# Performance work log

Hardware: AMD Instinct MI355X
Metric: run time of the kernel (lower is better)

The kernel has to match this reference:

```python
import jax, jax.numpy as jnp
import numpy as np

B, T, D = 2, 2048, 2048
H, HKV, HD = 16, 4, 128
I = 5632
EPS = 1e-5


def setup_inputs() -> dict:
    ks = jax.random.split(jax.random.key(0), 12)
    s = 0.02
    return {
        "x": jax.random.normal(ks[0], (B, T, D), jnp.float32),
        "rope_cos": jax.random.uniform(ks[1], (T, HD // 2), jnp.float32),
        "rope_sin": jax.random.uniform(ks[2], (T, HD // 2), jnp.float32),
        "ln1_w": jnp.ones((D,), jnp.float32),
        "ln2_w": jnp.ones((D,), jnp.float32),
        "wq_w": jax.random.normal(ks[3], (D, H * HD), jnp.float32) * s,
        "wq_b": jnp.zeros((H * HD,), jnp.float32),
        "wk_w": jax.random.normal(ks[4], (D, HKV * HD), jnp.float32) * s,
        "wk_b": jnp.zeros((HKV * HD,), jnp.float32),
        "wv_w": jax.random.normal(ks[5], (D, HKV * HD), jnp.float32) * s,
        "wv_b": jnp.zeros((HKV * HD,), jnp.float32),
        "wo_w": jax.random.normal(ks[6], (H * HD, D), jnp.float32) * s,
        "wo_b": jnp.zeros((D,), jnp.float32),
        "w1_w": jax.random.normal(ks[7], (D, 2 * I), jnp.float32) * s,
        "w1_b": jnp.zeros((2 * I,), jnp.float32),
        "w2_w": jax.random.normal(ks[8], (I, D), jnp.float32) * s,
        "w2_b": jnp.zeros((D,), jnp.float32),
    }


def _rmsnorm(x, w):
    return x * jax.lax.rsqrt(jnp.mean(x * x, axis=-1, keepdims=True) + EPS) * w


def _rotate(x, cos, sin):
    # x: [B, h, T, HD]; cos/sin: [T, HD/2] broadcast over [B, h, T, HD/2]
    x1, x2 = x[..., ::2], x[..., 1::2]
    return jnp.stack([x1 * cos - x2 * sin, x1 * sin + x2 * cos], axis=-1).reshape(x.shape)


def reference(x, rope_cos, rope_sin, ln1_w, ln2_w, wq_w, wq_b, wk_w, wk_b,
              wv_w, wv_b, wo_w, wo_b, w1_w, w1_b, w2_w, w2_b):
    h = _rmsnorm(x, ln1_w)
    q = (h @ wq_w + wq_b).reshape(B, T, H, HD).transpose(0, 2, 1, 3)
    k = (h @ wk_w + wk_b).reshape(B, T, HKV, HD).transpose(0, 2, 1, 3)
    v = (h @ wv_w + wv_b).reshape(B, T, HKV, HD).transpose(0, 2, 1, 3)
    q = _rotate(q, rope_cos, rope_sin)
    k = _rotate(k, rope_cos, rope_sin)
    rep = H // HKV
    k = jnp.repeat(k, rep, axis=1)  # GQA repeat_interleave over head dim
    v = jnp.repeat(v, rep, axis=1)
    scale = 1.0 / np.sqrt(HD).astype(np.float32)
    scores = jnp.einsum('bhqd,bhkd->bhqk', q, k) * scale  # [B,H,T,T]
    causal = jnp.tril(jnp.ones((T, T), bool))
    scores = jnp.where(causal, scores, -jnp.inf)
    attn = jax.nn.softmax(scores, axis=-1)
    out = jnp.einsum('bhqk,bhkd->bhqd', attn, v)
    out = out.transpose(0, 2, 1, 3).reshape(B, T, H * HD) @ wo_w + wo_b
    h1 = x + out
    g = _rmsnorm(h1, ln2_w)
    gate_up = g @ w1_w + w1_b
    gate, up = gate_up[..., :I], gate_up[..., I:]
    mlp = (jax.nn.silu(gate) * up) @ w2_w + w2_b
    return h1 + mlp
```

## Files before the change

### kernel.cpp

```cpp
#include <hip/hip_runtime.h>

#define T_SEQ 2048
#define DMODEL 2048
#define NH 16
#define NKV 4
#define HD 128
#define ISZ 5632
#define BATCH 2
#define QKS 2560

typedef unsigned short ushort_t;
typedef __attribute__((ext_vector_type(8))) short short8;
typedef __attribute__((ext_vector_type(4))) float f32x4;

__device__ __forceinline__ ushort_t f2bf(float f) {
  unsigned int u = __float_as_uint(f);
  unsigned int r = (u + 0x7FFFu + ((u >> 16) & 1u)) >> 16;
  return (ushort_t)r;
}
__device__ __forceinline__ float bf2f(ushort_t h) {
  return __uint_as_float(((unsigned int)h) << 16);
}

__global__ __launch_bounds__(256) void wconv_kernel(const float* __restrict__ W,
                                                    ushort_t* __restrict__ Wt,
                                                    int K, int N) {
  __shared__ float tile[32][33];
  const int n0 = blockIdx.x * 32, k0 = blockIdx.y * 32;
  const int t = threadIdx.x;
  const int r = t >> 3, c = (t & 7) * 4;
  float4 v = *(const float4*)(W + (size_t)(k0 + r) * N + n0 + c);
  tile[r][c + 0] = v.x; tile[r][c + 1] = v.y; tile[r][c + 2] = v.z; tile[r][c + 3] = v.w;
  __syncthreads();
  ushort4 o;
  o.x = f2bf(tile[c + 0][r]);
  o.y = f2bf(tile[c + 1][r]);
  o.z = f2bf(tile[c + 2][r]);
  o.w = f2bf(tile[c + 3][r]);
  *(ushort4*)(Wt + (size_t)(n0 + r) * K + k0 + c) = o;
}

__global__ __launch_bounds__(256) void catbias_kernel(const float* __restrict__ a,
                                                      const float* __restrict__ b,
                                                      float* __restrict__ o) {
  int i = blockIdx.x * 256 + threadIdx.x;
  if (i < QKS) o[i] = (i < 2048) ? a[i] : b[i - 2048];
}

__global__ __launch_bounds__(256) void rmsnorm_kernel(const float* __restrict__ x,
                                                      const float* __restrict__ w,
                                                      ushort_t* __restrict__ out) {
  const int row = blockIdx.x;
  const int t = threadIdx.x;
  const float* xr = x + (size_t)row * DMODEL;
  float4 v0 = *(const float4*)(xr + t * 4);
  float4 v1 = *(const float4*)(xr + 1024 + t * 4);
  float ss = v0.x * v0.x + v0.y * v0.y + v0.z * v0.z + v0.w * v0.w +
             v1.x * v1.x + v1.y * v1.y + v1.z * v1.z + v1.w * v1.w;
  #pragma unroll
  for (int m = 1; m < 64; m <<= 1) ss += __shfl_xor(ss, m);
  __shared__ float red[4];
  if ((t & 63) == 0) red[t >> 6] = ss;
  __syncthreads();
  float tot = red[0] + red[1] + red[2] + red[3];
  float rinv = rsqrtf(tot * (1.0f / DMODEL) + 1e-5f);
  float4 w0 = *(const float4*)(w + t * 4);
  float4 w1 = *(const float4*)(w + 1024 + t * 4);
  ushort4 o0, o1;
  o0.x = f2bf(v0.x * rinv * w0.x); o0.y = f2bf(v0.y * rinv * w0.y);
  o0.z = f2bf(v0.z * rinv * w0.z); o0.w = f2bf(v0.w * rinv * w0.w);
  o1.x = f2bf(v1.x * rinv * w1.x); o1.y = f2bf(v1.y * rinv * w1.y);
  o1.z = f2bf(v1.z * rinv * w1.z); o1.w = f2bf(v1.w * rinv * w1.w);
  *(ushort4*)(out + (size_t)row * DMODEL + t * 4) = o0;
  *(ushort4*)(out + (size_t)row * DMODEL + 1024 + t * 4) = o1;
}

__global__ __launch_bounds__(256) void rope_kernel(ushort_t* __restrict__ buf,
                                                   const float* __restrict__ cs,
                                                   const float* __restrict__ sn) {
  size_t idx = (size_t)blockIdx.x * 256 + threadIdx.x;
  int d = (int)(idx & 63);
  size_t rest = idx >> 6;
  int hh = (int)(rest % 20);
  size_t bt = rest / 20;
  int t = (int)(bt & (T_SEQ - 1));
  ushort_t* p = buf + bt * QKS + hh * HD + 2 * d;
  float x1 = bf2f(p[0]), x2 = bf2f(p[1]);
  float c = cs[t * 64 + d], s = sn[t * 64 + d];
  p[0] = f2bf(x1 * c - x2 * s);
  p[1] = f2bf(x1 * s + x2 * c);
}

__global__ __launch_bounds__(256) void swiglu_kernel(ushort_t* __restrict__ gu) {
  size_t i = (size_t)blockIdx.x * 256 + threadIdx.x;
  size_t m = i / (ISZ / 8);
  size_t j = (i % (ISZ / 8)) * 8;
  ushort_t* pg = gu + m * (2 * ISZ) + j;
  short8 gg = *(const short8*)pg;
  short8 uu = *(const short8*)(pg + ISZ);
  short8 oo;
  #pragma unroll
  for (int q = 0; q < 8; ++q) {
    float gv = bf2f((ushort_t)gg[q]);
    float uv = bf2f((ushort_t)uu[q]);
    float sl = gv / (1.f + __expf(-gv));
    oo[q] = (short)f2bf(sl * uv);
  }
  *(short8*)pg = oo;
}

__global__ __launch_bounds__(512, 2)
void gemm256_kernel(const ushort_t* __restrict__ A, int lda,
                    const ushort_t* __restrict__ Bt,
                    const float* __restrict__ bias, void* __restrict__ outp,
                    int M, int N, int K) {
  __shared__ ushort_t lds[65536];
  const int tid = threadIdx.x;
  const int wid = tid >> 6, lane = tid & 63;
  const int lq = lane & 15, g = lane >> 4;
  const int wm = wid >> 2, wn = wid & 3;
  const int m0 = blockIdx.x * 256, n0 = blockIdx.y * 256;

  const char* ldsc = (const char*)lds;
  const int c0 = ((g ^ (lq & 3)) << 4) | (((lq >> 2) & 1) << 6);
  const int rbA = wm * 8192 + lq * 128 + c0;
  const int rbAx = rbA ^ 64;
  const int rbB = 32768 + wn * 4096 + lq * 128 + c0;
  const int rbBx = rbB ^ 64;

  const int l3 = lane >> 3;
  const int clog = ((lane & 7) ^ l3) << 4;
  const int s0 = wid * 16 + l3, s1 = s0 + 8;
  const int rA0 = (s0 & 63) + ((s0 >> 6) << 7);
  const int rA0b = (s1 & 63) + ((s1 >> 6) << 7);
  const int rB0 = ((s0 >> 5) << 6) + (s0 & 31);
  const int rB0b = ((s1 >> 5) << 6) + (s1 & 31);
  const char* pA0a = (const char*)A + (size_t)(m0 + rA0) * (lda * 2) + clog;
  const char* pA0b = (const char*)A + (size_t)(m0 + rA0b) * (lda * 2) + clog;
  const char* pA1a = pA0a + (size_t)64 * (lda * 2);
  const char* pA1b = pA0b + (size_t)64 * (lda * 2);
  const char* pB0a = (const char*)Bt + (size_t)(n0 + rB0) * (K * 2) + clog;
  const char* pB0b = (const char*)Bt + (size_t)(n0 + rB0b) * (K * 2) + clog;
  const char* pB1a = pB0a + (size_t)32 * (K * 2);
  const char* pB1b = pB0b + (size_t)32 * (K * 2);
  ushort_t* sd = lds + wid * 1024;

#define GLL(SRC, DOFF)                                                        \
  __builtin_amdgcn_global_load_lds(                                           \
      (const __attribute__((address_space(1))) void*)(SRC),                   \
      (__attribute__((address_space(3))) void*)(sd + (DOFF)), 16, 0, 0)
#define STG_ALL(PB)                                                           \
  {                                                                           \
    GLL(pA0a, (PB)*32768 + 0);     GLL(pA0b, (PB)*32768 + 512);               \
    GLL(pB0a, (PB)*32768 + 16384); GLL(pB0b, (PB)*32768 + 16896);             \
    GLL(pB1a, (PB)*32768 + 24576); GLL(pB1b, (PB)*32768 + 25088);             \
    GLL(pA1a, (PB)*32768 + 8192);  GLL(pA1b, (PB)*32768 + 8704);              \
    pA0a += 128; pA0b += 128; pA1a += 128; pA1b += 128;                       \
    pB0a += 128; pB0b += 128; pB1a += 128; pB1b += 128;                       \
  }

  f32x4 acc[8][4] = {};

#define TILE(P, DOST)                                                         \
  {                                                                           \
    asm volatile("s_waitcnt vmcnt(0)" ::: "memory");                          \
    __builtin_amdgcn_s_barrier();                                             \
    if (DOST) STG_ALL((P) ^ 1)                                                \
    short8 aA0[4][2], aA1[4][2], bb0[2][2], bb1[2][2];                        \
    _Pragma("unroll") for (int mi = 0; mi < 4; ++mi) {                        \
      aA0[mi][0] = *(const short8*)(ldsc + (P)*65536 + rbA + mi * 2048);      \
      aA0[mi][1] = *(const short8*)(ldsc + (P)*65536 + rbAx + mi * 2048);     \
    }                                                                         \
    _Pragma("unroll") for (int nj = 0; nj < 2; ++nj) {                        \
      bb0[nj][0] = *(const short8*)(ldsc + (P)*65536 + rbB + nj * 2048);      \
      bb0[nj][1] = *(const short8*)(ldsc + (P)*65536 + rbBx + nj * 2048);     \
    }                                                                         \
    _Pragma("unroll") for (int mi = 0; mi < 4; ++mi)                          \
      _Pragma("unroll") for (int nj = 0; nj < 2; ++nj) {                      \
        acc[mi][nj] = __builtin_amdgcn_mfma_f32_16x16x32_bf16(aA0[mi][0], bb0[nj][0], acc[mi][nj], 0, 0, 0); \
        acc[mi][nj] = __builtin_amdgcn_mfma_f32_16x16x32_bf16(aA0[mi][1], bb0[nj][1], acc[mi][nj], 0, 0, 0); \
      }                                                                       \
    _Pragma("unroll") for (int nj = 0; nj < 2; ++nj) {                        \
      bb1[nj][0] = *(const short8*)(ldsc + (P)*65536 + rbB + 16384 + nj * 2048);  \
      bb1[nj][1] = *(const short8*)(ldsc + (P)*65536 + rbBx + 16384 + nj * 2048); \
    }                                                                         \
    _Pragma("unroll") for (int mi = 0; mi < 4; ++mi)                          \
      _Pragma("unroll") for (int nj = 0; nj < 2; ++nj) {                      \
        acc[mi][2 + nj] = __builtin_amdgcn_mfma_f32_16x16x32_bf16(aA0[mi][0], bb1[nj][0], acc[mi][2 + nj], 0, 0, 0); \
        acc[mi][2 + nj] = __builtin_amdgcn_mfma_f32_16x16x32_bf16(aA0[mi][1], bb1[nj][1], acc[mi][2 + nj], 0, 0, 0); \
      }                                                                       \
    _Pragma("unroll") for (int mi = 0; mi < 4; ++mi) {                        \
      aA1[mi][0] = *(const short8*)(ldsc + (P)*65536 + rbA + 16384 + mi * 2048);  \
      aA1[mi][1] = *(const short8*)(ldsc + (P)*65536 + rbAx + 16384 + mi * 2048); \
    }                                                                         \
    _Pragma("unroll") for (int mi = 0; mi < 4; ++mi)                          \
      _Pragma("unroll") for (int nj = 0; nj < 2; ++nj) {                      \
        acc[4 + mi][nj] = __builtin_amdgcn_mfma_f32_16x16x32_bf16(aA1[mi][0], bb0[nj][0], acc[4 + mi][nj], 0, 0, 0); \
        acc[4 + mi][nj] = __builtin_amdgcn_mfma_f32_16x16x32_bf16(aA1[mi][1], bb0[nj][1], acc[4 + mi][nj], 0, 0, 0); \
      }                                                                       \
    _Pragma("unroll") for (int mi = 0; mi < 4; ++mi)                          \
      _Pragma("unroll") for (int nj = 0; nj < 2; ++nj) {                      \
        acc[4 + mi][2 + nj] = __builtin_amdgcn_mfma_f32_16x16x32_bf16(aA1[mi][0], bb1[nj][0], acc[4 + mi][2 + nj], 0, 0, 0); \
        acc[4 + mi][2 + nj] = __builtin_amdgcn_mfma_f32_16x16x32_bf16(aA1[mi][1], bb1[nj][1], acc[4 + mi][2 + nj], 0, 0, 0); \
      }                                                                       \
  }

  STG_ALL(0)
  for (int it = 0; it < 15; ++it) {
    TILE(0, true)
    TILE(1, true)
  }
  TILE(0, true)
  TILE(1, false)
#undef TILE
#undef GLL
#undef STG_ALL

  #pragma unroll
  for (int nf = 0; nf < 4; ++nf) {
    int c = n0 + wn * 64 + nf * 16 + lq;
    float bb = bias[c];
    #pragma unroll
    for (int mf = 0; mf < 8; ++mf) {
      #pragma unroll
      for (int i = 0; i < 4; ++i) {
        int r = m0 + wm * 128 + mf * 16 + g * 4 + i;
        ((ushort_t*)outp)[(size_t)r * N + c] = f2bf(acc[mf][nf][i] + bb);
      }
    }
  }
}

__global__ __launch_bounds__(512, 1)
void gemm128_kernel(const ushort_t* __restrict__ A, int lda,
                    const ushort_t* __restrict__ Bt,
                    const float* __restrict__ bias, const float* __restrict__ res,
                    float* __restrict__ outp, int M, int N, int K) {
  __shared__ ushort_t lds[49152];
  const int tid = threadIdx.x;
  const int wid = tid >> 6, lane = tid & 63;
  const int lq = lane & 15, g = lane >> 4;
  const int wm = wid & 1, wn = wid >> 1;
  const int m0 = blockIdx.x * 128, n0 = blockIdx.y * 256;
  const int NT = K >> 6;

  const char* ldsc = (const char*)lds;
  const int c0 = ((g ^ (lq & 3)) << 4) | (((lq >> 2) & 1) << 6);
  const int rbA = wm * 8192 + lq * 128 + c0;
  const int rbAx = rbA ^ 64;
  const int rbB = 16384 + wn * 8192 + lq * 128 + c0;
  const int rbBx = rbB ^ 64;

  const char* pA[2];
  const char* pB[4];
  #pragma unroll
  for (int j = 0; j < 2; ++j) {
    int pb = (wid * 2 + j) * 1024 + lane * 16;
    int ob = pb ^ (((pb >> 7) & 7) << 4);
    pA[j] = (const char*)A + (size_t)(m0 + (ob >> 7)) * (lda * 2) + (ob & 127);
  }
  #pragma unroll
  for (int j = 0; j < 4; ++j) {
    int pb = (wid * 4 + j) * 1024 + lane * 16;
    int ob = pb ^ (((pb >> 7) & 7) << 4);
    pB[j] = (const char*)Bt + (size_t)(n0 + (ob >> 7)) * (K * 2) + (ob & 127);
  }
  ushort_t* sdA = lds + wid * 1024;
  ushort_t* sdB = lds + 8192 + wid * 2048;

#define GLL1(SRC, DST)                                                        \
  __builtin_amdgcn_global_load_lds(                                           \
      (const __attribute__((address_space(1))) void*)(SRC),                   \
      (__attribute__((address_space(3))) void*)(DST), 16, 0, 0)
#define STG128(PB)                                                            \
  {                                                                           \
    GLL1(pA[0], sdA + (PB)*24576 + 0);   GLL1(pA[1], sdA + (PB)*24576 + 512); \
    GLL1(pB[0], sdB + (PB)*24576 + 0);   GLL1(pB[1], sdB + (PB)*24576 + 512); \
    GLL1(pB[2], sdB + (PB)*24576 + 1024); GLL1(pB[3], sdB + (PB)*24576 + 1536); \
    pA[0] += 128; pA[1] += 128;                                               \
    pB[0] += 128; pB[1] += 128; pB[2] += 128; pB[3] += 128;                   \
  }

  f32x4 acc[4][4] = {};

#define TILE128(P, TCUR)                                                      \
  {                                                                           \
    asm volatile("s_waitcnt vmcnt(0)" ::: "memory");                          \
    __builtin_amdgcn_s_barrier();                                             \
    if ((TCUR) + 1 < NT) STG128((P) ^ 1)                                      \
    short8 aA[4][2], bb[4][2];                                                \
    _Pragma("unroll") for (int mi = 0; mi < 4; ++mi) {                        \
      aA[mi][0] = *(const short8*)(ldsc + (P)*49152 + rbA + mi * 2048);       \
      aA[mi][1] = *(const short8*)(ldsc + (P)*49152 + rbAx + mi * 2048);      \
    }                                                                         \
    _Pragma("unroll") for (int nj = 0; nj < 4; ++nj) {                        \
      bb[nj][0] = *(const short8*)(ldsc + (P)*49152 + rbB + nj * 2048);       \
      bb[nj][1] = *(const short8*)(ldsc + (P)*49152 + rbBx + nj * 2048);      \
    }                                                                         \
    _Pragma("unroll") for (int mi = 0; mi < 4; ++mi)                          \
      _Pragma("unroll") for (int nj = 0; nj < 4; ++nj) {                      \
        acc[mi][nj] = __builtin_amdgcn_mfma_f32_16x16x32_bf16(aA[mi][0], bb[nj][0], acc[mi][nj], 0, 0, 0); \
        acc[mi][nj] = __builtin_amdgcn_mfma_f32_16x16x32_bf16(aA[mi][1], bb[nj][1], acc[mi][nj], 0, 0, 0); \
      }                                                                       \
  }

  STG128(0)
  for (int t = 0; t < NT; t += 2) {
    TILE128(0, t)
    TILE128(1, t + 1)
  }
#undef TILE128
#undef GLL1
#undef STG128

  #pragma unroll
  for (int nf = 0; nf < 4; ++nf) {
    int c = n0 + wn * 64 + nf * 16 + lq;
    float bb = bias[c];
    #pragma unroll
    for (int mf = 0; mf < 4; ++mf) {
      #pragma unroll
      for (int i = 0; i < 4; ++i) {
        int r = m0 + wm * 64 + mf * 16 + g * 4 + i;
        size_t oidx = (size_t)r * N + c;
        outp[oidx] = res[oidx] + acc[mf][nf][i] + bb;
      }
    }
  }
}

#define BM 128
#define BN 128
#define BK 32

template <int MODE>
__global__ __launch_bounds__(256, 2)
void gemm_kernel(const ushort_t* __restrict__ A, int lda, const ushort_t* __restrict__ Bt,
                 const float* __restrict__ bias, const float* __restrict__ res,
                 void* __restrict__ outp, int M, int N, int K) {
  __shared__ ushort_t Alds[BM * BK];
  __shared__ ushort_t Blds[BM * BK];
  const int tid = threadIdx.x;
  const int w = tid >> 6, lane = tid & 63;
  const int lq = lane & 15, g = lane >> 4;
  const int m0 = blockIdx.y * BM, n0 = blockIdx.x * BN;
  const int ro = (w >> 1) * 64, co = (w & 1) * 64;

  f32x4 acc[4][4] = {};

  for (int k0 = 0; k0 < K; k0 += BK) {
    const ushort_t* ga = A + (size_t)m0 * lda + k0;
    const ushort_t* gb = Bt + (size_t)n0 * K + k0;
    #pragma unroll
    for (int it = 0; it < 2; ++it) {
      int ch = it * 256 + tid;
      int row = ch >> 2, cir = ch & 3;
      int lbase = (it * 256 + w * 64) * 8;
      __builtin_amdgcn_global_load_lds(
          (const __attribute__((address_space(1))) void*)(ga + (size_t)row * lda + cir * 8),
          (__attribute__((address_space(3))) void*)(&Alds[lbase]), 16, 0, 0);
      __builtin_amdgcn_global_load_lds(
          (const __attribute__((address_space(1))) void*)(gb + (size_t)row * K + cir * 8),
          (__attribute__((address_space(3))) void*)(&Blds[lbase]), 16, 0, 0);
    }
    __syncthreads();
    short8 af[4], br[4];
    #pragma unroll
    for (int mi = 0; mi < 4; ++mi)
      af[mi] = *(const short8*)(&Alds[(ro + mi * 16 + lq) * BK + g * 8]);
    #pragma unroll
    for (int ni = 0; ni < 4; ++ni)
      br[ni] = *(const short8*)(&Blds[(co + ni * 16 + lq) * BK + g * 8]);
    #pragma unroll
    for (int mi = 0; mi < 4; ++mi)
      #pragma unroll
      for (int ni = 0; ni < 4; ++ni)
        acc[mi][ni] = __builtin_amdgcn_mfma_f32_16x16x32_bf16(af[mi], br[ni], acc[mi][ni], 0, 0, 0);
    __syncthreads();
  }

  #pragma unroll
  for (int ni = 0; ni < 4; ++ni) {
    int c = n0 + co + ni * 16 + lq;
    float bb = bias[c];
    #pragma unroll
    for (int mi = 0; mi < 4; ++mi) {
      #pragma unroll
      for (int i = 0; i < 4; ++i) {
        int r = m0 + ro + mi * 16 + g * 4 + i;
        size_t oidx = (size_t)r * N + c;
        float av = acc[mi][ni][i] + bb;
        if (MODE == 1) {
          ((float*)outp)[oidx] = res[oidx] + av;
        } else {
          int b2 = r >> 11, t2 = r & (T_SEQ - 1);
          int hk = c >> 7, dd = c & (HD - 1);
          ((ushort_t*)outp)[((size_t)(b2 * NKV + hk) * HD + dd) * T_SEQ + t2] = f2bf(av);
        }
      }
    }
  }
}

#define QB 128
#define KB 64
#define PSTR 72

__global__ __launch_bounds__(256, 2)
void attn_kernel(const ushort_t* __restrict__ qk, const ushort_t* __restrict__ vT,
                 ushort_t* __restrict__ ao) {
  __shared__ ushort_t Klds[KB * 128];
  __shared__ ushort_t Vlds[HD * 64];
  __shared__ ushort_t Plds[4][16 * PSTR];

  const int tid = threadIdx.x;
  const int w = tid >> 6, lane = tid & 63;
  const int lq = lane & 15, g = lane >> 4;
  const int nqb = T_SEQ / QB;
  const int xq = blockIdx.x;
  const int qi = (xq & 1) ? (nqb - 1 - (xq >> 1)) : (xq >> 1);
  const int qb = qi * QB;
  const int h = blockIdx.y;
  const int b = blockIdx.z;
  const int hkv = h >> 2;
  const float scale = 0.08838834764831845f;

  short8 qf[2][4];
  #pragma unroll
  for (int gi = 0; gi < 2; ++gi) {
    const ushort_t* qrow = qk + ((size_t)(b * T_SEQ + qb + gi * 64 + w * 16 + lq) * QKS) + h * HD;
    #pragma unroll
    for (int ks = 0; ks < 4; ++ks) qf[gi][ks] = *(const short8*)(qrow + ks * 32 + g * 8);
  }

  f32x4 of[2][8] = {};
  float m_run[2] = {-1e30f, -1e30f};
  float l_run[2] = {0.f, 0.f};

  const char* kbaseC = (const char*)(qk + (size_t)b * T_SEQ * QKS + 2048 + hkv * HD);
  const char* vbaseC = (const char*)(vT + (size_t)(b * NKV + hkv) * HD * T_SEQ);
  const char* pK[4];
  const char* pV[4];
  #pragma unroll
  for (int j = 0; j < 4; ++j) {
    int krow = w * 16 + j * 4 + (lane >> 4);
    int kcol = ((lane & 15) * 16) ^ ((krow & 7) << 4);
    pK[j] = kbaseC + (size_t)krow * (QKS * 2) + kcol;
    int vrow = w * 32 + j * 8 + (lane >> 3);
    int vcol = ((lane & 7) * 16) ^ ((vrow & 7) << 4);
    pV[j] = vbaseC + (size_t)vrow * (T_SEQ * 2) + vcol;
  }
  ushort_t* kdst = Klds + w * 2048;
  ushort_t* vdst = Vlds + w * 2048;
  const char* kldsC = (const char*)Klds;
  const char* vldsC = (const char*)Vlds;

#define AGLL(SRC, DST)                                                        \
  __builtin_amdgcn_global_load_lds(                                           \
      (const __attribute__((address_space(1))) void*)(SRC),                   \
      (__attribute__((address_space(3))) void*)(DST), 16, 0, 0)

  const int nt = qb / KB + 2;
  for (int ti = 0; ti < nt; ++ti) {
    const int kt = ti * KB;
    #pragma unroll
    for (int j = 0; j < 4; ++j) {
      AGLL(pK[j], kdst + j * 512);
      AGLL(pV[j], vdst + j * 512);
      pK[j] += (size_t)KB * (QKS * 2);
      pV[j] += KB * 2;
    }
    asm volatile("s_waitcnt vmcnt(0)" ::: "memory");
    __builtin_amdgcn_s_barrier();

    #pragma unroll
    for (int gi = 0; gi < 2; ++gi) {
      const int qw = qb + gi * 64 + w * 16;
      if (kt <= qw + 15) {
        f32x4 s[4] = {};
        __builtin_amdgcn_s_setprio(1);
        #pragma unroll
        for (int c = 0; c < 4; ++c) {
          int krow = c * 16 + lq;
          #pragma unroll
          for (int ks = 0; ks < 4; ++ks) {
            short8 kf = *(const short8*)(kldsC + krow * 256 + (((ks * 64) + g * 16) ^ ((krow & 7) << 4)));
            s[c] = __builtin_amdgcn_mfma_f32_16x16x32_bf16(kf, qf[gi][ks], s[c], 0, 0, 0);
          }
        }
        __builtin_amdgcn_s_setprio(0);
        const int qg = qw + lq;
        float sv[16];
        #pragma unroll
        for (int c = 0; c < 4; ++c)
          #pragma unroll
          for (int i = 0; i < 4; ++i) {
            int kvg = kt + c * 16 + 4 * g + i;
            float xx = s[c][i] * scale;
            sv[c * 4 + i] = (kvg > qg) ? -1e30f : xx;
          }
        float tmax = sv[0];
        #pragma unroll
        for (int j = 1; j < 16; ++j) tmax = fmaxf(tmax, sv[j]);
        tmax = fmaxf(tmax, __shfl_xor(tmax, 16));
        tmax = fmaxf(tmax, __shfl_xor(tmax, 32));
        float mnew = fmaxf(m_run[gi], tmax);
        float corr = __expf(m_run[gi] - mnew);
        float pv[16];
        float ps = 0.f;
        #pragma unroll
        for (int j = 0; j < 16; ++j) { pv[j] = __expf(sv[j] - mnew); ps += pv[j]; }
        ps += __shfl_xor(ps, 16);
        ps += __shfl_xor(ps, 32);
        l_run[gi] = l_run[gi] * corr + ps;
        m_run[gi] = mnew;
        float c4[4];
        #pragma unroll
        for (int i = 0; i < 4; ++i) c4[i] = __shfl(corr, 4 * g + i);
        #pragma unroll
        for (int n = 0; n < 8; ++n)
          #pragma unroll
          for (int i = 0; i < 4; ++i) of[gi][n][i] *= c4[i];
        #pragma unroll
        for (int c = 0; c < 4; ++c) {
          ushort4 pw;
          pw.x = f2bf(pv[c * 4 + 0]); pw.y = f2bf(pv[c * 4 + 1]);
          pw.z = f2bf(pv[c * 4 + 2]); pw.w = f2bf(pv[c * 4 + 3]);
          *(ushort4*)(&Plds[w][lq * PSTR + c * 16 + 4 * g]) = pw;
        }
        short8 pf0 = *(const short8*)(&Plds[w][lq * PSTR + g * 8]);
        short8 pf1 = *(const short8*)(&Plds[w][lq * PSTR + 32 + g * 8]);
        __builtin_amdgcn_s_setprio(1);
        #pragma unroll
        for (int n = 0; n < 8; ++n) {
          int vr = n * 16 + lq;
          short8 vf0 = *(const short8*)(vldsC + vr * 128 + ((g * 16) ^ ((vr & 7) << 4)));
          short8 vf1 = *(const short8*)(vldsC + vr * 128 + ((64 + g * 16) ^ ((vr & 7) << 4)));
          of[gi][n] = __builtin_amdgcn_mfma_f32_16x16x32_bf16(pf0, vf0, of[gi][n], 0, 0, 0);
          of[gi][n] = __builtin_amdgcn_mfma_f32_16x16x32_bf16(pf1, vf1, of[gi][n], 0, 0, 0);
        }
        __builtin_amdgcn_s_setprio(0);
      }
    }
    __builtin_amdgcn_s_barrier();
  }
#undef AGLL

  #pragma unroll
  for (int gi = 0; gi < 2; ++gi) {
    float li[4];
    #pragma unroll
    for (int i = 0; i < 4; ++i) li[i] = 1.f / __shfl(l_run[gi], 4 * g + i);
    #pragma unroll
    for (int n = 0; n < 8; ++n)
      #pragma unroll
      for (int i = 0; i < 4; ++i) {
        int tok = qb + gi * 64 + w * 16 + 4 * g + i;
        ao[((size_t)(b * T_SEQ + tok) * (NH * HD)) + h * HD + n * 16 + lq] = f2bf(of[gi][n][i] * li[i]);
      }
  }
}

extern "C" void kernel_launch(void* const* d_in, const int* in_sizes, int n_in,
                              void* d_out, int out_size, void* d_ws, size_t ws_size,
                              hipStream_t stream) {
  const float* x   = (const float*)d_in[0];
  const float* rc  = (const float*)d_in[1];
  const float* rs  = (const float*)d_in[2];
  const float* ln1 = (const float*)d_in[3];
  const float* ln2 = (const float*)d_in[4];
  const float* wq  = (const float*)d_in[5];
  const float* wqb = (const float*)d_in[6];
  const float* wk  = (const float*)d_in[7];
  const float* wkb = (const float*)d_in[8];
  const float* wv  = (const float*)d_in[9];
  const float* wvb = (const float*)d_in[10];
  const float* wo  = (const float*)d_in[11];
  const float* wob = (const float*)d_in[12];
  const float* w1  = (const float*)d_in[13];
  const float* w1b = (const float*)d_in[14];
  const float* w2  = (const float*)d_in[15];
  const float* w2b = (const float*)d_in[16];

  char* ws = (char*)d_ws;
  size_t off = 0;
  auto alloc = [&](size_t bytes) {
    char* p = ws + off;
    off += (bytes + 255) & ~(size_t)255;
    return (void*)p;
  };
  const int M = BATCH * T_SEQ;
  ushort_t* w1T  = (ushort_t*)alloc((size_t)11264 * 2048 * 2);
  ushort_t* w2T  = (ushort_t*)alloc((size_t)2048 * 5632 * 2);
  ushort_t* hbuf = (ushort_t*)alloc((size_t)M * 2048 * 2);
  ushort_t* vbufT= (ushort_t*)alloc((size_t)M * 512 * 2);
  float*    qkb  = (float*)alloc((size_t)QKS * 4);
  size_t guStart = off;
  ushort_t* wqkT = (ushort_t*)alloc((size_t)QKS * 2048 * 2);
  ushort_t* wvT  = (ushort_t*)alloc((size_t)512 * 2048 * 2);
  ushort_t* woT  = (ushort_t*)alloc((size_t)2048 * 2048 * 2);
  ushort_t* qkbuf= (ushort_t*)alloc((size_t)M * QKS * 2);
  size_t guBytes = (size_t)M * 11264 * 2;
  size_t used = off - guStart;
  if (guBytes > used) alloc(guBytes - used);
  ushort_t* gu = (ushort_t*)(ws + guStart);
  float* h1 = (float*)d_out;
  if (off > ws_size) return;

  wconv_kernel<<<dim3(2048 / 32, 2048 / 32), 256, 0, stream>>>(wq, wqkT, 2048, 2048);
  wconv_kernel<<<dim3(512 / 32, 2048 / 32), 256, 0, stream>>>(wk, wqkT + (size_t)2048 * 2048, 2048, 512);
  wconv_kernel<<<dim3(512 / 32, 2048 / 32), 256, 0, stream>>>(wv, wvT, 2048, 512);
  wconv_kernel<<<dim3(2048 / 32, 2048 / 32), 256, 0, stream>>>(wo, woT, 2048, 2048);
  wconv_kernel<<<dim3(11264 / 32, 2048 / 32), 256, 0, stream>>>(w1, w1T, 2048, 11264);
  wconv_kernel<<<dim3(2048 / 32, 5632 / 32), 256, 0, stream>>>(w2, w2T, 5632, 2048);
  catbias_kernel<<<10, 256, 0, stream>>>(wqb, wkb, qkb);

  rmsnorm_kernel<<<M, 256, 0, stream>>>(x, ln1, hbuf);

  gemm256_kernel<<<dim3(M / 256, QKS / 256), 512, 0, stream>>>(hbuf, 2048, wqkT, qkb, qkbuf, M, QKS, 2048);
  gemm_kernel<3><<<dim3(512 / BN, M / BM), 256, 0, stream>>>(hbuf, 2048, wvT, wvb, nullptr, vbufT, M, 512, 2048);

  rope_kernel<<<(M * 20 * 64) / 256, 256, 0, stream>>>(qkbuf, rc, rs);

  attn_kernel<<<dim3(T_SEQ / QB, NH, BATCH), 256, 0, stream>>>(qkbuf, vbufT, hbuf);

  gemm128_kernel<<<dim3(M / 128, 2048 / 256), 512, 0, stream>>>(hbuf, 2048, woT, wob, x, h1, M, 2048, 2048);

  rmsnorm_kernel<<<M, 256, 0, stream>>>(h1, ln2, hbuf);

  gemm256_kernel<<<dim3(M / 256, 11264 / 256), 512, 0, stream>>>(hbuf, 2048, w1T, w1b, gu, M, 11264, 2048);

  swiglu_kernel<<<(M * (ISZ / 8)) / 256, 256, 0, stream>>>(gu);

  gemm128_kernel<<<dim3(M / 128, 2048 / 256), 512, 0, stream>>>(gu, 11264, w2T, w2b, h1, (float*)d_out, M, 2048, 5632);

  (void)in_sizes; (void)n_in; (void)out_size;
}
```

Measured before the change: 663.2 us.

## Unify GEMMs into one 128x256 kernel with BK=32 and higher occupancy

Replaces the 256x256 and 128x256 (BK=64) GEMM kernels with a single templated 128x256 kernel that uses a K-step of 32, a smaller LDS footprint (48KB double-buffered), and launch bounds allowing 4 blocks per CU. The MODE template selects a bf16 output or an fp32 output with a residual add. The aim is more resident blocks and better latency hiding, and also more blocks in the grid for the QK and W1 GEMMs. In exchange it halves the work done per barrier, adds sync overhead per K step, and lowers per-block operand reuse for the large GEMMs.

```diff
diff --git a/kernel.cpp b/kernel.cpp
--- a/kernel.cpp
+++ b/kernel.cpp
@@ -109,209 +109,70 @@
   *(short8*)pg = oo;
 }
 
-__global__ __launch_bounds__(512, 2)
-void gemm256_kernel(const ushort_t* __restrict__ A, int lda,
-                    const ushort_t* __restrict__ Bt,
-                    const float* __restrict__ bias, void* __restrict__ outp,
-                    int M, int N, int K) {
-  __shared__ ushort_t lds[65536];
-  const int tid = threadIdx.x;
-  const int wid = tid >> 6, lane = tid & 63;
-  const int lq = lane & 15, g = lane >> 4;
-  const int wm = wid >> 2, wn = wid & 3;
-  const int m0 = blockIdx.x * 256, n0 = blockIdx.y * 256;
-
-  const char* ldsc = (const char*)lds;
-  const int c0 = ((g ^ (lq & 3)) << 4) | (((lq >> 2) & 1) << 6);
-  const int rbA = wm * 8192 + lq * 128 + c0;
-  const int rbAx = rbA ^ 64;
-  const int rbB = 32768 + wn * 4096 + lq * 128 + c0;
-  const int rbBx = rbB ^ 64;
-
-  const int l3 = lane >> 3;
-  const int clog = ((lane & 7) ^ l3) << 4;
-  const int s0 = wid * 16 + l3, s1 = s0 + 8;
-  const int rA0 = (s0 & 63) + ((s0 >> 6) << 7);
-  const int rA0b = (s1 & 63) + ((s1 >> 6) << 7);
-  const int rB0 = ((s0 >> 5) << 6) + (s0 & 31);
-  const int rB0b = ((s1 >> 5) << 6) + (s1 & 31);
-  const char* pA0a = (const char*)A + (size_t)(m0 + rA0) * (lda * 2) + clog;
-  const char* pA0b = (const char*)A + (size_t)(m0 + rA0b) * (lda * 2) + clog;
-  const char* pA1a = pA0a + (size_t)64 * (lda * 2);
-  const char* pA1b = pA0b + (size_t)64 * (lda * 2);
-  const char* pB0a = (const char*)Bt + (size_t)(n0 + rB0) * (K * 2) + clog;
-  const char* pB0b = (const char*)Bt + (size_t)(n0 + rB0b) * (K * 2) + clog;
-  const char* pB1a = pB0a + (size_t)32 * (K * 2);
-  const char* pB1b = pB0b + (size_t)32 * (K * 2);
-  ushort_t* sd = lds + wid * 1024;
-
-#define GLL(SRC, DOFF)                                                        \
-  __builtin_amdgcn_global_load_lds(                                           \
-      (const __attribute__((address_space(1))) void*)(SRC),                   \
-      (__attribute__((address_space(3))) void*)(sd + (DOFF)), 16, 0, 0)
-#define STG_ALL(PB)                                                           \
-  {                                                                           \
-    GLL(pA0a, (PB)*32768 + 0);     GLL(pA0b, (PB)*32768 + 512);               \
-    GLL(pB0a, (PB)*32768 + 16384); GLL(pB0b, (PB)*32768 + 16896);             \
-    GLL(pB1a, (PB)*32768 + 24576); GLL(pB1b, (PB)*32768 + 25088);             \
-    GLL(pA1a, (PB)*32768 + 8192);  GLL(pA1b, (PB)*32768 + 8704);              \
-    pA0a += 128; pA0b += 128; pA1a += 128; pA1b += 128;                       \
-    pB0a += 128; pB0b += 128; pB1a += 128; pB1b += 128;                       \
-  }
-
-  f32x4 acc[8][4] = {};
-
-#define TILE(P, DOST)                                                         \
-  {                                                                           \
-    asm volatile("s_waitcnt vmcnt(0)" ::: "memory");                          \
-    __builtin_amdgcn_s_barrier();                                             \
-    if (DOST) STG_ALL((P) ^ 1)                                                \
-    short8 aA0[4][2], aA1[4][2], bb0[2][2], bb1[2][2];                        \
-    _Pragma("unroll") for (int mi = 0; mi < 4; ++mi) {                        \
-      aA0[mi][0] = *(const short8*)(ldsc + (P)*65536 + rbA + mi * 2048);      \
-      aA0[mi][1] = *(const short8*)(ldsc + (P)*65536 + rbAx + mi * 2048);     \
-    }                                                                         \
-    _Pragma("unroll") for (int nj = 0; nj < 2; ++nj) {                        \
-      bb0[nj][0] = *(const short8*)(ldsc + (P)*65536 + rbB + nj * 2048);      \
-      bb0[nj][1] = *(const short8*)(ldsc + (P)*65536 + rbBx + nj * 2048);     \
-    }                                                                         \
-    _Pragma("unroll") for (int mi = 0; mi < 4; ++mi)                          \
-      _Pragma("unroll") for (int nj = 0; nj < 2; ++nj) {                      \
-        acc[mi][nj] = __builtin_amdgcn_mfma_f32_16x16x32_bf16(aA0[mi][0], bb0[nj][0], acc[mi][nj], 0, 0, 0); \
-        acc[mi][nj] = __builtin_amdgcn_mfma_f32_16x16x32_bf16(aA0[mi][1], bb0[nj][1], acc[mi][nj], 0, 0, 0); \
-      }                                                                       \
-    _Pragma("unroll") for (int nj = 0; nj < 2; ++nj) {                        \
-      bb1[nj][0] = *(const short8*)(ldsc + (P)*65536 + rbB + 16384 + nj * 2048);  \
-      bb1[nj][1] = *(const short8*)(ldsc + (P)*65536 + rbBx + 16384 + nj * 2048); \
-    }                                                                         \
-    _Pragma("unroll") for (int mi = 0; mi < 4; ++mi)                          \
-      _Pragma("unroll") for (int nj = 0; nj < 2; ++nj) {                      \
-        acc[mi][2 + nj] = __builtin_amdgcn_mfma_f32_16x16x32_bf16(aA0[mi][0], bb1[nj][0], acc[mi][2 + nj], 0, 0, 0); \
-        acc[mi][2 + nj] = __builtin_amdgcn_mfma_f32_16x16x32_bf16(aA0[mi][1], bb1[nj][1], acc[mi][2 + nj], 0, 0, 0); \
-      }                                                                       \
-    _Pragma("unroll") for (int mi = 0; mi < 4; ++mi) {                        \
-      aA1[mi][0] = *(const short8*)(ldsc + (P)*65536 + rbA + 16384 + mi * 2048);  \
-      aA1[mi][1] = *(const short8*)(ldsc + (P)*65536 + rbAx + 16384 + mi * 2048); \
-    }                                                                         \
-    _Pragma("unroll") for (int mi = 0; mi < 4; ++mi)                          \
-      _Pragma("unroll") for (int nj = 0; nj < 2; ++nj) {                      \
-        acc[4 + mi][nj] = __builtin_amdgcn_mfma_f32_16x16x32_bf16(aA1[mi][0], bb0[nj][0], acc[4 + mi][nj], 0, 0, 0); \
-        acc[4 + mi][nj] = __builtin_amdgcn_mfma_f32_16x16x32_bf16(aA1[mi][1], bb0[nj][1], acc[4 + mi][nj], 0, 0, 0); \
-      }                                                                       \
-    _Pragma("unroll") for (int mi = 0; mi < 4; ++mi)                          \
-      _Pragma("unroll") for (int nj = 0; nj < 2; ++nj) {                      \
-        acc[4 + mi][2 + nj] = __builtin_amdgcn_mfma_f32_16x16x32_bf16(aA1[mi][0], bb1[nj][0], acc[4 + mi][2 + nj], 0, 0, 0); \
-        acc[4 + mi][2 + nj] = __builtin_amdgcn_mfma_f32_16x16x32_bf16(aA1[mi][1], bb1[nj][1], acc[4 + mi][2 + nj], 0, 0, 0); \
-      }                                                                       \
-  }
-
-  STG_ALL(0)
-  for (int it = 0; it < 15; ++it) {
-    TILE(0, true)
-    TILE(1, true)
-  }
-  TILE(0, true)
-  TILE(1, false)
-#undef TILE
-#undef GLL
-#undef STG_ALL
-
-  #pragma unroll
-  for (int nf = 0; nf < 4; ++nf) {
-    int c = n0 + wn * 64 + nf * 16 + lq;
-    float bb = bias[c];
-    #pragma unroll
-    for (int mf = 0; mf < 8; ++mf) {
-      #pragma unroll
-      for (int i = 0; i < 4; ++i) {
-        int r = m0 + wm * 128 + mf * 16 + g * 4 + i;
-        ((ushort_t*)outp)[(size_t)r * N + c] = f2bf(acc[mf][nf][i] + bb);
-      }
-    }
-  }
-}
-
-__global__ __launch_bounds__(512, 1)
-void gemm128_kernel(const ushort_t* __restrict__ A, int lda,
-                    const ushort_t* __restrict__ Bt,
-                    const float* __restrict__ bias, const float* __restrict__ res,
-                    float* __restrict__ outp, int M, int N, int K) {
-  __shared__ ushort_t lds[49152];
+template <int MODE>
+__global__ __launch_bounds__(512, 4)
+void gemmW_kernel(const ushort_t* __restrict__ A, int lda,
+                  const ushort_t* __restrict__ Bt,
+                  const float* __restrict__ bias, const float* __restrict__ res,
+                  void* __restrict__ outp, int M, int N, int K) {
+  __shared__ ushort_t lds[24576];
   const int tid = threadIdx.x;
   const int wid = tid >> 6, lane = tid & 63;
   const int lq = lane & 15, g = lane >> 4;
   const int wm = wid & 1, wn = wid >> 1;
   const int m0 = blockIdx.x * 128, n0 = blockIdx.y * 256;
-  const int NT = K >> 6;
+  const int NT = K >> 5;
 
   const char* ldsc = (const char*)lds;
-  const int c0 = ((g ^ (lq & 3)) << 4) | (((lq >> 2) & 1) << 6);
-  const int rbA = wm * 8192 + lq * 128 + c0;
-  const int rbAx = rbA ^ 64;
-  const int rbB = 16384 + wn * 8192 + lq * 128 + c0;
-  const int rbBx = rbB ^ 64;
-
-  const char* pA[2];
-  const char* pB[4];
-  #pragma unroll
-  for (int j = 0; j < 2; ++j) {
-    int pb = (wid * 2 + j) * 1024 + lane * 16;
-    int ob = pb ^ (((pb >> 7) & 7) << 4);
-    pA[j] = (const char*)A + (size_t)(m0 + (ob >> 7)) * (lda * 2) + (ob & 127);
-  }
-  #pragma unroll
-  for (int j = 0; j < 4; ++j) {
-    int pb = (wid * 4 + j) * 1024 + lane * 16;
-    int ob = pb ^ (((pb >> 7) & 7) << 4);
-    pB[j] = (const char*)Bt + (size_t)(n0 + (ob >> 7)) * (K * 2) + (ob & 127);
-  }
-  ushort_t* sdA = lds + wid * 1024;
-  ushort_t* sdB = lds + 8192 + wid * 2048;
-
-#define GLL1(SRC, DST)                                                        \
+  const int c0 = ((g ^ ((lq >> 1) & 3)) << 4);
+  const int rbA = wm * 4096 + lq * 64 + c0;
+  const int rbB = 8192 + wn * 4096 + lq * 64 + c0;
+
+  const int rsrc = lane >> 2;
+  const int clog = (((lane & 3) ^ ((lane >> 3) & 3)) << 4);
+  const char* pAg  = (const char*)A + (size_t)(m0 + wid * 16 + rsrc) * (lda * 2) + clog;
+  const char* pBg0 = (const char*)Bt + (size_t)(n0 + wid * 32 + rsrc) * (K * 2) + clog;
+  const char* pBg1 = (const char*)Bt + (size_t)(n0 + wid * 32 + 16 + rsrc) * (K * 2) + clog;
+  ushort_t* sdA = lds + wid * 512;
+  ushort_t* sdB = lds + 4096 + wid * 1024;
+
+#define GLLW(SRC, DST)                                                        \
   __builtin_amdgcn_global_load_lds(                                           \
       (const __attribute__((address_space(1))) void*)(SRC),                   \
       (__attribute__((address_space(3))) void*)(DST), 16, 0, 0)
-#define STG128(PB)                                                            \
+#define STGW(PB)                                                              \
   {                                                                           \
-    GLL1(pA[0], sdA + (PB)*24576 + 0);   GLL1(pA[1], sdA + (PB)*24576 + 512); \
-    GLL1(pB[0], sdB + (PB)*24576 + 0);   GLL1(pB[1], sdB + (PB)*24576 + 512); \
-    GLL1(pB[2], sdB + (PB)*24576 + 1024); GLL1(pB[3], sdB + (PB)*24576 + 1536); \
-    pA[0] += 128; pA[1] += 128;                                               \
-    pB[0] += 128; pB[1] += 128; pB[2] += 128; pB[3] += 128;                   \
+    GLLW(pAg, sdA + (PB)*12288);                                              \
+    GLLW(pBg0, sdB + (PB)*12288);                                             \
+    GLLW(pBg1, sdB + (PB)*12288 + 512);                                       \
+    pAg += 64; pBg0 += 64; pBg1 += 64;                                        \
   }
 
   f32x4 acc[4][4] = {};
 
-#define TILE128(P, TCUR)                                                      \
+#define TILEW(P, TCUR)                                                        \
   {                                                                           \
     asm volatile("s_waitcnt vmcnt(0)" ::: "memory");                          \
     __builtin_amdgcn_s_barrier();                                             \
-    if ((TCUR) + 1 < NT) STG128((P) ^ 1)                                      \
-    short8 aA[4][2], bb[4][2];                                                \
-    _Pragma("unroll") for (int mi = 0; mi < 4; ++mi) {                        \
-      aA[mi][0] = *(const short8*)(ldsc + (P)*49152 + rbA + mi * 2048);       \
-      aA[mi][1] = *(const short8*)(ldsc + (P)*49152 + rbAx + mi * 2048);      \
-    }                                                                         \
-    _Pragma("unroll") for (int nj = 0; nj < 4; ++nj) {                        \
-      bb[nj][0] = *(const short8*)(ldsc + (P)*49152 + rbB + nj * 2048);       \
-      bb[nj][1] = *(const short8*)(ldsc + (P)*49152 + rbBx + nj * 2048);      \
-    }                                                                         \
+    if ((TCUR) + 1 < NT) STGW((P) ^ 1)                                        \
+    short8 aA[4], bb[4];                                                      \
     _Pragma("unroll") for (int mi = 0; mi < 4; ++mi)                          \
-      _Pragma("unroll") for (int nj = 0; nj < 4; ++nj) {                      \
-        acc[mi][nj] = __builtin_amdgcn_mfma_f32_16x16x32_bf16(aA[mi][0], bb[nj][0], acc[mi][nj], 0, 0, 0); \
-        acc[mi][nj] = __builtin_amdgcn_mfma_f32_16x16x32_bf16(aA[mi][1], bb[nj][1], acc[mi][nj], 0, 0, 0); \
-      }                                                                       \
-  }
-
-  STG128(0)
+      aA[mi] = *(const short8*)(ldsc + (P)*24576 + rbA + mi * 1024);          \
+    _Pragma("unroll") for (int nj = 0; nj < 4; ++nj)                          \
+      bb[nj] = *(const short8*)(ldsc + (P)*24576 + rbB + nj * 1024);          \
+    _Pragma("unroll") for (int mi = 0; mi < 4; ++mi)                          \
+      _Pragma("unroll") for (int nj = 0; nj < 4; ++nj)                        \
+        acc[mi][nj] = __builtin_amdgcn_mfma_f32_16x16x32_bf16(aA[mi], bb[nj], acc[mi][nj], 0, 0, 0); \
+  }
+
+  STGW(0)
   for (int t = 0; t < NT; t += 2) {
-    TILE128(0, t)
-    TILE128(1, t + 1)
-  }
-#undef TILE128
-#undef GLL1
-#undef STG128
+    TILEW(0, t)
+    TILEW(1, t + 1)
+  }
+#undef TILEW
+#undef GLLW
+#undef STGW
 
   #pragma unroll
   for (int nf = 0; nf < 4; ++nf) {
@@ -323,7 +184,12 @@
       for (int i = 0; i < 4; ++i) {
         int r = m0 + wm * 64 + mf * 16 + g * 4 + i;
         size_t oidx = (size_t)r * N + c;
-        outp[oidx] = res[oidx] + acc[mf][nf][i] + bb;
+        float av = acc[mf][nf][i] + bb;
+        if (MODE == 0) {
+          ((ushort_t*)outp)[oidx] = f2bf(av);
+        } else {
+          ((float*)outp)[oidx] = res[oidx] + av;
+        }
       }
     }
   }
@@ -617,22 +483,22 @@
 
   rmsnorm_kernel<<<M, 256, 0, stream>>>(x, ln1, hbuf);
 
-  gemm256_kernel<<<dim3(M / 256, QKS / 256), 512, 0, stream>>>(hbuf, 2048, wqkT, qkb, qkbuf, M, QKS, 2048);
+  gemmW_kernel<0><<<dim3(M / 128, QKS / 256), 512, 0, stream>>>(hbuf, 2048, wqkT, qkb, nullptr, qkbuf, M, QKS, 2048);
   gemm_kernel<3><<<dim3(512 / BN, M / BM), 256, 0, stream>>>(hbuf, 2048, wvT, wvb, nullptr, vbufT, M, 512, 2048);
 
   rope_kernel<<<(M * 20 * 64) / 256, 256, 0, stream>>>(qkbuf, rc, rs);
 
   attn_kernel<<<dim3(T_SEQ / QB, NH, BATCH), 256, 0, stream>>>(qkbuf, vbufT, hbuf);
 
-  gemm128_kernel<<<dim3(M / 128, 2048 / 256), 512, 0, stream>>>(hbuf, 2048, woT, wob, x, h1, M, 2048, 2048);
+  gemmW_kernel<1><<<dim3(M / 128, 2048 / 256), 512, 0, stream>>>(hbuf, 2048, woT, wob, x, h1, M, 2048, 2048);
 
   rmsnorm_kernel<<<M, 256, 0, stream>>>(h1, ln2, hbuf);
 
-  gemm256_kernel<<<dim3(M / 256, 11264 / 256), 512, 0, stream>>>(hbuf, 2048, w1T, w1b, gu, M, 11264, 2048);
+  gemmW_kernel<0><<<dim3(M / 128, 11264 / 256), 512, 0, stream>>>(hbuf, 2048, w1T, w1b, nullptr, gu, M, 11264, 2048);
 
   swiglu_kernel<<<(M * (ISZ / 8)) / 256, 256, 0, stream>>>(gu);
 
-  gemm128_kernel<<<dim3(M / 128, 2048 / 256), 512, 0, stream>>>(gu, 11264, w2T, w2b, h1, (float*)d_out, M, 2048, 5632);
+  gemmW_kernel<1><<<dim3(M / 128, 2048 / 256), 512, 0, stream>>>(gu, 11264, w2T, w2b, h1, (float*)d_out, M, 2048, 5632);
 
   (void)in_sizes; (void)n_in; (void)out_size;
 }
```

New measurement: 720.7 us. 1.09x slower.
